# Optimization experiments

Hardware: AMD Instinct MI355X
Metric: run time of the kernel (lower is better)

Reference implementation:

```python
import jax, jax.numpy as jnp
import numpy as np


def setup_inputs() -> dict:
    key = jax.random.key(0)
    k1, k2, k3 = jax.random.split(key, 3)
    B, N, M = 4, 8192, 8192
    xyz1 = jax.random.normal(k1, (B, N, 3), dtype=jnp.float32)
    xyz2 = jax.random.normal(k2, (B, M, 3), dtype=jnp.float32)
    weights1 = jax.random.uniform(k3, (B, N), dtype=jnp.float32)
    return {"xyz1": xyz1, "xyz2": xyz2, "weights1": weights1}


def _min_sqdist(xyz1, xyz2):
    n2 = jnp.sum(xyz1 * xyz1, axis=-1)  # [B,N]
    m2 = jnp.sum(xyz2 * xyz2, axis=-1)  # [B,M]
    cross = jnp.einsum("bnd,bmd->bnm", xyz1, xyz2)
    sq = n2[:, :, None] + m2[:, None, :] - 2.0 * cross
    sq = jnp.maximum(sq, 0.0)  # numerical clamp, matches exact squared dist >= 0
    return jnp.min(sq, axis=2)  # [B,N] nearest-neighbor squared distance


def reference(xyz1, xyz2, weights1) -> jnp.ndarray:
    # dist1: for each point in xyz1, squared distance to nearest point in xyz2
    dist1 = jnp.sqrt(_min_sqdist(xyz1, xyz2))  # [B,N] L1 (euclidean) distances
    dist1 = dist1 * weights1
    return jnp.sum(dist1) / jnp.sum(weights1)
```

## Files before the change

kernel.cpp:

```cpp
#include <hip/hip_runtime.h>
#include <math.h>

constexpr int B = 4;
constexpr int N = 8192;
constexpr int M = 8192;
constexpr int NPTS = B * N;
constexpr int MPTS = B * M;

constexpr int TPB = 256;
constexpr int PB  = 8;
constexpr int PTS_PER_BLOCK = TPB * PB;
constexpr int NB1 = N / PTS_PER_BLOCK;
constexpr int MC  = 64;
constexpr int CHUNK = M / MC;

constexpr int RB = 128;

typedef float v2f __attribute__((ext_vector_type(2)));

__global__ __launch_bounds__(TPB, 4) void chamfer_min_kernel(
    const float* __restrict__ xyz1, const float* __restrict__ xyz2,
    float* __restrict__ part) {
  __shared__ float lqx[CHUNK], lqy[CHUNK], lqz[CHUNK], lqw[CHUNK];

  const int t  = threadIdx.x;
  const int mc = blockIdx.x;
  const int pb = blockIdx.y;
  const int b  = blockIdx.z;

  if (t < CHUNK) {
    int gi = b * M + mc * CHUNK + t;
    float x = xyz2[3 * gi + 0];
    float y = xyz2[3 * gi + 1];
    float z = xyz2[3 * gi + 2];
    lqx[t] = -2.0f * x;
    lqy[t] = -2.0f * y;
    lqz[t] = -2.0f * z;
    lqw[t] = fmaf(x, x, fmaf(y, y, z * z));
  }

  v2f x1b[PB], y1b[PB], z1b[PB];
  float smin[PB];
  const int base1 = b * N + pb * PTS_PER_BLOCK + t;
#pragma unroll
  for (int p = 0; p < PB; ++p) {
    int idx = base1 + p * TPB;
    float x = xyz1[3 * idx + 0];
    float y = xyz1[3 * idx + 1];
    float z = xyz1[3 * idx + 2];
    x1b[p] = (v2f){x, x};
    y1b[p] = (v2f){y, y};
    z1b[p] = (v2f){z, z};
    smin[p] = INFINITY;
  }
  __syncthreads();

#pragma unroll 4
  for (int j4 = 0; j4 < CHUNK / 4; ++j4) {
    float4 vx = *(const float4*)&lqx[4 * j4];
    float4 vy = *(const float4*)&lqy[4 * j4];
    float4 vz = *(const float4*)&lqz[4 * j4];
    float4 vw = *(const float4*)&lqw[4 * j4];

    v2f px0 = (v2f){vx.x, vx.y}, px1 = (v2f){vx.z, vx.w};
    v2f py0 = (v2f){vy.x, vy.y}, py1 = (v2f){vy.z, vy.w};
    v2f pz0 = (v2f){vz.x, vz.y}, pz1 = (v2f){vz.z, vz.w};
    v2f pw0 = (v2f){vw.x, vw.y}, pw1 = (v2f){vw.z, vw.w};

#pragma unroll
    for (int p = 0; p < PB; ++p) {
      v2f s0 = __builtin_elementwise_fma(
          x1b[p], px0,
          __builtin_elementwise_fma(
              y1b[p], py0, __builtin_elementwise_fma(z1b[p], pz0, pw0)));
      smin[p] = fminf(fminf(s0.x, s0.y), smin[p]);
      v2f s1 = __builtin_elementwise_fma(
          x1b[p], px1,
          __builtin_elementwise_fma(
              y1b[p], py1, __builtin_elementwise_fma(z1b[p], pz1, pw1)));
      smin[p] = fminf(fminf(s1.x, s1.y), smin[p]);
    }
  }

#pragma unroll
  for (int p = 0; p < PB; ++p) {
    int idx = base1 + p * TPB;
    float x = x1b[p].x, y = y1b[p].x, z = z1b[p].x;
    float n2 = fmaf(x, x, fmaf(y, y, z * z));
    float d2 = fmaxf(n2 + smin[p], 0.0f);
    part[(size_t)mc * NPTS + idx] = d2;
  }
}

__global__ __launch_bounds__(TPB) void reduce_kernel(
    const float* __restrict__ part, const float* __restrict__ w,
    float* __restrict__ pnum, float* __restrict__ pden) {
  int i = blockIdx.x * TPB + threadIdx.x;

  float m0 = INFINITY, m1 = INFINITY, m2 = INFINITY, m3 = INFINITY;
#pragma unroll
  for (int mc = 0; mc < MC; mc += 4) {
    m0 = fminf(m0, part[(size_t)(mc + 0) * NPTS + i]);
    m1 = fminf(m1, part[(size_t)(mc + 1) * NPTS + i]);
    m2 = fminf(m2, part[(size_t)(mc + 2) * NPTS + i]);
    m3 = fminf(m3, part[(size_t)(mc + 3) * NPTS + i]);
  }
  float d  = sqrtf(fminf(fminf(m0, m1), fminf(m2, m3)));
  float wi = w[i];
  float num = d * wi;
  float den = wi;

#pragma unroll
  for (int off = 32; off > 0; off >>= 1) {
    num += __shfl_down(num, off, 64);
    den += __shfl_down(den, off, 64);
  }

  __shared__ float snum[TPB / 64], sden[TPB / 64];
  int wid  = threadIdx.x >> 6;
  int lane = threadIdx.x & 63;
  if (lane == 0) { snum[wid] = num; sden[wid] = den; }
  __syncthreads();
  if (threadIdx.x == 0) {
    float a = 0.0f, c = 0.0f;
#pragma unroll
    for (int k = 0; k < TPB / 64; ++k) { a += snum[k]; c += sden[k]; }
    pnum[blockIdx.x] = a;
    pden[blockIdx.x] = c;
  }
}

__global__ __launch_bounds__(RB) void finalize_kernel(
    const float* __restrict__ pnum, const float* __restrict__ pden,
    float* __restrict__ out) {
  int t = threadIdx.x;
  float num = pnum[t];
  float den = pden[t];
#pragma unroll
  for (int off = 32; off > 0; off >>= 1) {
    num += __shfl_down(num, off, 64);
    den += __shfl_down(den, off, 64);
  }
  __shared__ float sn[2], sd[2];
  if ((t & 63) == 0) { sn[t >> 6] = num; sd[t >> 6] = den; }
  __syncthreads();
  if (t == 0) out[0] = (sn[0] + sn[1]) / (sd[0] + sd[1]);
}

extern "C" void kernel_launch(void* const* d_in, const int* in_sizes, int n_in,
                              void* d_out, int out_size, void* d_ws,
                              size_t ws_size, hipStream_t stream) {
  const float* xyz1 = (const float*)d_in[0];
  const float* xyz2 = (const float*)d_in[1];
  const float* wts  = (const float*)d_in[2];
  float* out = (float*)d_out;

  char* ws = (char*)d_ws;
  float* part = (float*)ws;
  float* pnum = (float*)(ws + (size_t)MC * NPTS * sizeof(float));
  float* pden = pnum + RB;

  hipLaunchKernelGGL(chamfer_min_kernel, dim3(MC, NB1, B), dim3(TPB), 0,
                     stream, xyz1, xyz2, part);
  hipLaunchKernelGGL(reduce_kernel, dim3(NPTS / TPB), dim3(TPB), 0, stream,
                     part, wts, pnum, pden);
  hipLaunchKernelGGL(finalize_kernel, dim3(1), dim3(RB), 0, stream, pnum, pden,
                     out);
}
```

Measured before the change: 90.67 us.

## Double points per thread and fuse finalize into reduce via atomic last-block

Raises points per thread from 8 to 16 with launch bounds relaxed to 2 blocks per CU, so each LDS query load is reused across more points and the grid halves. The separate finalize kernel is removed: reduce blocks atomically add their partial sums and a counter, and the last block writes the final ratio. Accumulators are zeroed by the first thread of the min kernel. This saves one launch and adds register pressure and a lower occupancy limit, and the atomic float order makes the result non-deterministic.

```diff
diff --git a/kernel.cpp b/kernel.cpp
--- a/kernel.cpp
+++ b/kernel.cpp
@@ -8,25 +8,32 @@
 constexpr int MPTS = B * M;
 
 constexpr int TPB = 256;
-constexpr int PB  = 8;
+constexpr int PB  = 16;
 constexpr int PTS_PER_BLOCK = TPB * PB;
 constexpr int NB1 = N / PTS_PER_BLOCK;
 constexpr int MC  = 64;
 constexpr int CHUNK = M / MC;
 
-constexpr int RB = 128;
+constexpr int RBLOCKS = NPTS / TPB;
 
 typedef float v2f __attribute__((ext_vector_type(2)));
 
-__global__ __launch_bounds__(TPB, 4) void chamfer_min_kernel(
+__global__ __launch_bounds__(TPB, 2) void chamfer_min_kernel(
     const float* __restrict__ xyz1, const float* __restrict__ xyz2,
-    float* __restrict__ part) {
+    float* __restrict__ part, float* __restrict__ acc,
+    unsigned* __restrict__ counter) {
   __shared__ float lqx[CHUNK], lqy[CHUNK], lqz[CHUNK], lqw[CHUNK];
 
   const int t  = threadIdx.x;
   const int mc = blockIdx.x;
   const int pb = blockIdx.y;
   const int b  = blockIdx.z;
+
+  if (mc == 0 && pb == 0 && b == 0 && t == 0) {
+    acc[0] = 0.0f;
+    acc[1] = 0.0f;
+    counter[0] = 0u;
+  }
 
   if (t < CHUNK) {
     int gi = b * M + mc * CHUNK + t;
@@ -39,7 +46,7 @@
     lqw[t] = fmaf(x, x, fmaf(y, y, z * z));
   }
 
-  v2f x1b[PB], y1b[PB], z1b[PB];
+  v2f x2[PB], y2[PB], z2[PB];
   float smin[PB];
   const int base1 = b * N + pb * PTS_PER_BLOCK + t;
 #pragma unroll
@@ -48,9 +55,9 @@
     float x = xyz1[3 * idx + 0];
     float y = xyz1[3 * idx + 1];
     float z = xyz1[3 * idx + 2];
-    x1b[p] = (v2f){x, x};
-    y1b[p] = (v2f){y, y};
-    z1b[p] = (v2f){z, z};
+    x2[p] = (v2f){x, x};
+    y2[p] = (v2f){y, y};
+    z2[p] = (v2f){z, z};
     smin[p] = INFINITY;
   }
   __syncthreads();
@@ -62,22 +69,22 @@
     float4 vz = *(const float4*)&lqz[4 * j4];
     float4 vw = *(const float4*)&lqw[4 * j4];
 
-    v2f px0 = (v2f){vx.x, vx.y}, px1 = (v2f){vx.z, vx.w};
-    v2f py0 = (v2f){vy.x, vy.y}, py1 = (v2f){vy.z, vy.w};
-    v2f pz0 = (v2f){vz.x, vz.y}, pz1 = (v2f){vz.z, vz.w};
-    v2f pw0 = (v2f){vw.x, vw.y}, pw1 = (v2f){vw.z, vw.w};
+    v2f qx0 = (v2f){vx.x, vx.y}, qx1 = (v2f){vx.z, vx.w};
+    v2f qy0 = (v2f){vy.x, vy.y}, qy1 = (v2f){vy.z, vy.w};
+    v2f qz0 = (v2f){vz.x, vz.y}, qz1 = (v2f){vz.z, vz.w};
+    v2f qw0 = (v2f){vw.x, vw.y}, qw1 = (v2f){vw.z, vw.w};
 
 #pragma unroll
     for (int p = 0; p < PB; ++p) {
       v2f s0 = __builtin_elementwise_fma(
-          x1b[p], px0,
+          x2[p], qx0,
           __builtin_elementwise_fma(
-              y1b[p], py0, __builtin_elementwise_fma(z1b[p], pz0, pw0)));
+              y2[p], qy0, __builtin_elementwise_fma(z2[p], qz0, qw0)));
       smin[p] = fminf(fminf(s0.x, s0.y), smin[p]);
       v2f s1 = __builtin_elementwise_fma(
-          x1b[p], px1,
+          x2[p], qx1,
           __builtin_elementwise_fma(
-              y1b[p], py1, __builtin_elementwise_fma(z1b[p], pz1, pw1)));
+              y2[p], qy1, __builtin_elementwise_fma(z2[p], qz1, qw1)));
       smin[p] = fminf(fminf(s1.x, s1.y), smin[p]);
     }
   }
@@ -85,27 +92,30 @@
 #pragma unroll
   for (int p = 0; p < PB; ++p) {
     int idx = base1 + p * TPB;
-    float x = x1b[p].x, y = y1b[p].x, z = z1b[p].x;
+    float x = x2[p].x, y = y2[p].x, z = z2[p].x;
     float n2 = fmaf(x, x, fmaf(y, y, z * z));
-    float d2 = fmaxf(n2 + smin[p], 0.0f);
-    part[(size_t)mc * NPTS + idx] = d2;
+    part[(size_t)mc * NPTS + idx] = fmaxf(n2 + smin[p], 0.0f);
   }
 }
 
-__global__ __launch_bounds__(TPB) void reduce_kernel(
+__global__ __launch_bounds__(TPB) void reduce_finalize_kernel(
     const float* __restrict__ part, const float* __restrict__ w,
-    float* __restrict__ pnum, float* __restrict__ pden) {
-  int i = blockIdx.x * TPB + threadIdx.x;
+    float* __restrict__ acc, unsigned* __restrict__ counter,
+    float* __restrict__ out) {
+  const int i = blockIdx.x * TPB + threadIdx.x;
 
-  float m0 = INFINITY, m1 = INFINITY, m2 = INFINITY, m3 = INFINITY;
+  float m[8];
 #pragma unroll
-  for (int mc = 0; mc < MC; mc += 4) {
-    m0 = fminf(m0, part[(size_t)(mc + 0) * NPTS + i]);
-    m1 = fminf(m1, part[(size_t)(mc + 1) * NPTS + i]);
-    m2 = fminf(m2, part[(size_t)(mc + 2) * NPTS + i]);
-    m3 = fminf(m3, part[(size_t)(mc + 3) * NPTS + i]);
+  for (int k = 0; k < 8; ++k) m[k] = INFINITY;
+#pragma unroll
+  for (int mc = 0; mc < MC; mc += 8) {
+#pragma unroll
+    for (int k = 0; k < 8; ++k)
+      m[k] = fminf(m[k], part[(size_t)(mc + k) * NPTS + i]);
   }
-  float d  = sqrtf(fminf(fminf(m0, m1), fminf(m2, m3)));
+  float d2 = fminf(fminf(fminf(m[0], m[1]), fminf(m[2], m[3])),
+                   fminf(fminf(m[4], m[5]), fminf(m[6], m[7])));
+  float d  = sqrtf(d2);
   float wi = w[i];
   float num = d * wi;
   float den = wi;
@@ -117,34 +127,25 @@
   }
 
   __shared__ float snum[TPB / 64], sden[TPB / 64];
-  int wid  = threadIdx.x >> 6;
-  int lane = threadIdx.x & 63;
+  const int wid  = threadIdx.x >> 6;
+  const int lane = threadIdx.x & 63;
   if (lane == 0) { snum[wid] = num; sden[wid] = den; }
   __syncthreads();
+
   if (threadIdx.x == 0) {
     float a = 0.0f, c = 0.0f;
 #pragma unroll
     for (int k = 0; k < TPB / 64; ++k) { a += snum[k]; c += sden[k]; }
-    pnum[blockIdx.x] = a;
-    pden[blockIdx.x] = c;
+    atomicAdd(&acc[0], a);
+    atomicAdd(&acc[1], c);
+    __threadfence();
+    unsigned prev = atomicAdd(counter, 1u);
+    if (prev == (unsigned)(gridDim.x - 1)) {
+      float ta = atomicAdd(&acc[0], 0.0f);
+      float tc = atomicAdd(&acc[1], 0.0f);
+      out[0] = ta / tc;
+    }
   }
-}
-
-__global__ __launch_bounds__(RB) void finalize_kernel(
-    const float* __restrict__ pnum, const float* __restrict__ pden,
-    float* __restrict__ out) {
-  int t = threadIdx.x;
-  float num = pnum[t];
-  float den = pden[t];
-#pragma unroll
-  for (int off = 32; off > 0; off >>= 1) {
-    num += __shfl_down(num, off, 64);
-    den += __shfl_down(den, off, 64);
-  }
-  __shared__ float sn[2], sd[2];
-  if ((t & 63) == 0) { sn[t >> 6] = num; sd[t >> 6] = den; }
-  __syncthreads();
-  if (t == 0) out[0] = (sn[0] + sn[1]) / (sd[0] + sd[1]);
 }
 
 extern "C" void kernel_launch(void* const* d_in, const int* in_sizes, int n_in,
@@ -156,14 +157,12 @@
   float* out = (float*)d_out;
 
   char* ws = (char*)d_ws;
-  float* part = (float*)ws;
-  float* pnum = (float*)(ws + (size_t)MC * NPTS * sizeof(float));
-  float* pden = pnum + RB;
+  float*    part    = (float*)ws;
+  float*    acc     = (float*)(ws + (size_t)MC * NPTS * sizeof(float));
+  unsigned* counter = (unsigned*)(acc + 2);
 
   hipLaunchKernelGGL(chamfer_min_kernel, dim3(MC, NB1, B), dim3(TPB), 0,
-                     stream, xyz1, xyz2, part);
-  hipLaunchKernelGGL(reduce_kernel, dim3(NPTS / TPB), dim3(TPB), 0, stream,
-                     part, wts, pnum, pden);
-  hipLaunchKernelGGL(finalize_kernel, dim3(1), dim3(RB), 0, stream, pnum, pden,
-                     out);
+                     stream, xyz1, xyz2, part, acc, counter);
+  hipLaunchKernelGGL(reduce_finalize_kernel, dim3(RBLOCKS), dim3(TPB), 0,
+                     stream, part, wts, acc, counter, out);
 }
```

Result: faster. 87.54 us (-3.5%).
